# Kernel tuning notes

Measured on AMD Instinct MI355X. Metric: run time of the kernel, lower is better.

## Reference

```python
import jax, jax.numpy as jnp
import numpy as np

B, N_PER, F = 8, 4096, 64
RATIO, RADIUS, K = 0.25, 0.2, 64
S = int(N_PER * RATIO)  # 1024 samples per cloud
NEG = -1e30


def setup_inputs() -> dict:
    key = jax.random.key(0)
    ks = jax.random.split(key, 8)
    pos = jax.random.uniform(ks[0], (B * N_PER, 3), dtype=jnp.float32)
    x = jax.random.normal(ks[1], (B * N_PER, F), dtype=jnp.float32)
    batch = jnp.repeat(jnp.arange(B, dtype=jnp.int32), N_PER)
    W1 = jax.random.normal(ks[2], (F + 3, 128), dtype=jnp.float32) * 0.05
    b1 = jnp.zeros((128,), jnp.float32)
    W2 = jax.random.normal(ks[3], (128, 128), dtype=jnp.float32) * 0.05
    b2 = jnp.zeros((128,), jnp.float32)
    W3 = jax.random.normal(ks[4], (128, 256), dtype=jnp.float32) * 0.05
    b3 = jnp.zeros((256,), jnp.float32)
    return {"x": x, "pos": pos, "batch": batch,
            "W1": W1, "b1": b1, "W2": W2, "b2": b2, "W3": W3, "b3": b3}


def _fps_single(p):
    """Farthest point sampling on one cloud p:[N,3] -> S int32 indices (seed idx 0)."""
    d0 = jnp.sum((p - p[0]) ** 2, axis=-1)  # [N]

    def step(min_d, _):
        nxt = jnp.argmax(min_d).astype(jnp.int32)
        d = jnp.sum((p - p[nxt]) ** 2, axis=-1)
        return jnp.minimum(min_d, d), nxt

    _, rest = jax.lax.scan(step, d0, None, length=S - 1)
    return jnp.concatenate([jnp.zeros((1,), jnp.int32), rest])


def reference(x, pos, batch, W1, b1, W2, b2, W3, b3):
    pos_b = pos.reshape(B, N_PER, 3)
    x_b = x.reshape(B, N_PER, F)
    batch_b = batch.reshape(B, N_PER)

    # --- FPS sampling (sequential scan, vmapped over clouds) ---
    idx = jax.vmap(_fps_single)(pos_b)                                  # [B,S]
    pos_s = jnp.take_along_axis(pos_b, idx[..., None], axis=1)          # [B,S,3]

    # --- radius neighbor search: nearest K within RADIUS (deterministic) ---
    d2 = jnp.sum((pos_s[:, :, None, :] - pos_b[:, None, :, :]) ** 2, -1)  # [B,S,N]
    neg = jnp.where(d2 <= RADIUS ** 2, -d2, NEG)
    vals, nbr = jax.lax.top_k(neg, K)                                   # [B,S,K]
    valid = vals > NEG / 2                                              # [B,S,K]

    # --- gather neighbor features / positions ---
    x_j = jnp.take_along_axis(x_b[:, None], nbr[..., None], axis=2)     # [B,S,K,F]
    pos_j = jnp.take_along_axis(pos_b[:, None], nbr[..., None], axis=2) # [B,S,K,3]
    rel = pos_j - pos_s[:, :, None, :]                                  # [B,S,K,3]

    # --- edge MLP (Lin+ReLU per PyG PointNetConv local_nn) ---
    h = jnp.concatenate([x_j, rel], axis=-1)                            # [B,S,K,F+3]
    h = jax.nn.relu(h @ W1 + b1)
    h = jax.nn.relu(h @ W2 + b2)
    h = jax.nn.relu(h @ W3 + b3)                                        # [B,S,K,256]

    # --- scatter-max aggregation over neighbors ---
    h = jnp.where(valid[..., None], h, NEG)
    out = jnp.max(h, axis=2)                                            # [B,S,256]
    out = jnp.where(out > NEG / 2, out, 0.0)

    x1 = out.reshape(B * S, -1)
    pos1 = pos_s.reshape(B * S, 3)
    batch1 = jnp.take_along_axis(batch_b, idx, axis=1).reshape(-1)
    return x1, pos1, batch1
```

## Files before the change

kernel.cpp:

```cpp
#include <hip/hip_runtime.h>
#include <hip/hip_bf16.h>
#include <stdint.h>

#define NPER 4096
#define NCLOUD 8
#define FD 64
#define SS 1024
#define NBK 64
#define CAP 512

typedef unsigned int u32;
typedef unsigned long long u64;
typedef __attribute__((ext_vector_type(8))) short short8v;
typedef __attribute__((ext_vector_type(8))) unsigned short ushort8v;
typedef __attribute__((ext_vector_type(4))) float f32x4;

__device__ __forceinline__ float fadd(float a, float b){ return __fadd_rn(a,b); }
__device__ __forceinline__ float fsub(float a, float b){ return __fsub_rn(a,b); }
__device__ __forceinline__ float fmul(float a, float b){ return __fmul_rn(a,b); }
__device__ __forceinline__ float dist2(float ax,float ay,float az,float bx,float by,float bz){
  float dx=fsub(ax,bx), dy=fsub(ay,by), dz=fsub(az,bz);
  return fadd(fadd(fmul(dx,dx),fmul(dy,dy)),fmul(dz,dz));
}
__device__ __forceinline__ unsigned short f2b(float v){
  __hip_bfloat16 h = __float2bfloat16(v);
  return *reinterpret_cast<unsigned short*>(&h);
}

template<int CTRL, int RMASK>
__device__ __forceinline__ float dppmaxf(float v){
  int t = __builtin_amdgcn_update_dpp(0, __float_as_int(v), CTRL, RMASK, 0xf, false);
  return fmaxf(v, __int_as_float(t));
}

#define LOADG(q, j0, j1, j2, j3) { \
    const float4* pv = (const float4*)(pb + (size_t)(base + q*4)*3); \
    float4 v0=pv[0], v1=pv[1], v2=pv[2]; \
    x##j0=v0.x; y##j0=v0.y; z##j0=v0.z; \
    x##j1=v0.w; y##j1=v1.x; z##j1=v1.y; \
    x##j2=v1.z; y##j2=v1.w; z##j2=v2.x; \
    x##j3=v2.y; y##j3=v2.z; z##j3=v2.w; \
    float4 c0; c0.x=x##j0; c0.y=y##j0; c0.z=z##j0; c0.w=0.f; spt[base+q*4+0]=c0; \
    float4 c1; c1.x=x##j1; c1.y=y##j1; c1.z=z##j1; c1.w=0.f; spt[base+q*4+1]=c1; \
    float4 c2; c2.x=x##j2; c2.y=y##j2; c2.z=z##j2; c2.w=0.f; spt[base+q*4+2]=c2; \
    float4 c3; c3.x=x##j3; c3.y=y##j3; c3.z=z##j3; c3.w=0.f; spt[base+q*4+3]=c3; \
  }
#define DINIT(j) m##j = dist2(x##j,y##j,z##j,p0x,p0y,p0z);
#define DUPD(j)  { float d = dist2(x##j,y##j,z##j,pnx,pny,pnz); m##j = fminf(m##j,d); }
#define ARGMAX16() { \
      bool c; float w0,w1,w2,w3,w4,w5,w6,w7; int i0,i1,i2,i3,i4,i5,i6,i7; \
      c=m1>m0;   w0=c?m1:m0;   i0=base+(c?1:0); \
      c=m3>m2;   w1=c?m3:m2;   i1=base+(c?3:2); \
      c=m5>m4;   w2=c?m5:m4;   i2=base+(c?5:4); \
      c=m7>m6;   w3=c?m7:m6;   i3=base+(c?7:6); \
      c=m9>m8;   w4=c?m9:m8;   i4=base+(c?9:8); \
      c=m11>m10; w5=c?m11:m10; i5=base+(c?11:10); \
      c=m13>m12; w6=c?m13:m12; i6=base+(c?13:12); \
      c=m15>m14; w7=c?m15:m14; i7=base+(c?15:14); \
      c=w1>w0; w0=c?w1:w0; i0=c?i1:i0; \
      c=w3>w2; w2=c?w3:w2; i2=c?i3:i2; \
      c=w5>w4; w4=c?w5:w4; i4=c?i5:i4; \
      c=w7>w6; w6=c?w7:w6; i6=c?i7:i6; \
      c=w2>w0; w0=c?w2:w0; i0=c?i2:i0; \
      c=w6>w4; w4=c?w6:w4; i4=c?i6:i4; \
      c=w4>w0; bv=c?w4:w0; bidx=c?i4:i0; \
    }

__global__ __launch_bounds__(256, 1) void k_fps(const float* __restrict__ pos,
    float* __restrict__ pos_s, float* __restrict__ out_pos1, float* __restrict__ out_b1){
  __shared__ __align__(16) float4 spt[NPER];
  __shared__ __align__(16) u64 skey[2][4];
  const int b = blockIdx.x;
  const int t = threadIdx.x;
  const int w = t >> 6, lane = t & 63;
  const float* pb = pos + (size_t)b*NPER*3;
  const int base = t*16;
  float x0,x1,x2,x3,x4,x5,x6,x7,x8,x9,x10,x11,x12,x13,x14,x15;
  float y0,y1,y2,y3,y4,y5,y6,y7,y8,y9,y10,y11,y12,y13,y14,y15;
  float z0,z1,z2,z3,z4,z5,z6,z7,z8,z9,z10,z11,z12,z13,z14,z15;
  float m0,m1,m2,m3,m4,m5,m6,m7,m8,m9,m10,m11,m12,m13,m14,m15;
  LOADG(0, 0, 1, 2, 3)
  LOADG(1, 4, 5, 6, 7)
  LOADG(2, 8, 9, 10, 11)
  LOADG(3, 12, 13, 14, 15)
  const float p0x=pb[0], p0y=pb[1], p0z=pb[2];
  DINIT(0) DINIT(1) DINIT(2) DINIT(3) DINIT(4) DINIT(5) DINIT(6) DINIT(7)
  DINIT(8) DINIT(9) DINIT(10) DINIT(11) DINIT(12) DINIT(13) DINIT(14) DINIT(15)
  float bv; int bidx;
  ARGMAX16()
  float wx0=p0x, wy0=p0y, wz0=p0z;
  float wx1=0.f, wy1=0.f, wz1=0.f;
  float wx2=0.f, wy2=0.f, wz2=0.f;
  float wx3=0.f, wy3=0.f, wz3=0.f;
  for (int i=t;i<SS;i+=256) out_b1[b*SS+i] = (float)b;
  __syncthreads();
  auto fps_iter = [&](int it, float& wx, float& wy, float& wz) __attribute__((always_inline)) {
    float rv = bv;
    rv = dppmaxf<0x121,0xf>(rv);
    rv = dppmaxf<0x122,0xf>(rv);
    rv = dppmaxf<0x124,0xf>(rv);
    rv = dppmaxf<0x128,0xf>(rv);
    rv = dppmaxf<0x142,0xa>(rv);
    rv = dppmaxf<0x143,0xc>(rv);
    const float wv = __int_as_float(__builtin_amdgcn_readlane(__float_as_int(rv), 63));
    u64 em  = __ballot(bv == wv);
    u64 jb0 = __ballot((bidx & 1) != 0);
    u64 jb1 = __ballot((bidx & 2) != 0);
    u64 jb2 = __ballot((bidx & 4) != 0);
    u64 jb3 = __ballot((bidx & 8) != 0);
    const int wl = __ffsll(em) - 1;
    const int j  = (int)((jb0>>wl)&1) | ((int)((jb1>>wl)&1)<<1)
                 | ((int)((jb2>>wl)&1)<<2) | ((int)((jb3>>wl)&1)<<3);
    const int widx = (((w<<6)+wl)<<4) | j;
    const int par = it & 1;
    if (lane == 0)
      skey[par][w] = ((u64)__float_as_uint(wv)<<32) | (u64)(u32)(4095 - widx);
    __syncthreads();
    const u64* kp = &skey[par][0];
    u64 k0=kp[0], k1=kp[1], k2=kp[2], k3=kp[3];
    u64 ka = k0>k1?k0:k1, kb2 = k2>k3?k2:k3;
    u64 km = ka>kb2?ka:kb2;
    const int nxt = 4095 - (int)(km & 0xFFFull);
    const float4 c = spt[nxt];
    const float pnx = __int_as_float(__builtin_amdgcn_readfirstlane(__float_as_int(c.x)));
    const float pny = __int_as_float(__builtin_amdgcn_readfirstlane(__float_as_int(c.y)));
    const float pnz = __int_as_float(__builtin_amdgcn_readfirstlane(__float_as_int(c.z)));
    const bool mine = (t == (it & 255));
    wx = mine ? pnx : wx;
    wy = mine ? pny : wy;
    wz = mine ? pnz : wz;
    DUPD(0) DUPD(1) DUPD(2) DUPD(3) DUPD(4) DUPD(5) DUPD(6) DUPD(7)
    DUPD(8) DUPD(9) DUPD(10) DUPD(11) DUPD(12) DUPD(13) DUPD(14) DUPD(15)
    ARGMAX16()
  };
  for (int it=1;   it<256;  ++it) fps_iter(it, wx0, wy0, wz0);
  for (int it=256; it<512;  ++it) fps_iter(it, wx1, wy1, wz1);
  for (int it=512; it<768;  ++it) fps_iter(it, wx2, wy2, wz2);
  for (int it=768; it<1024; ++it) fps_iter(it, wx3, wy3, wz3);
  {
    const size_t g = (size_t)b*SS;
    size_t o = (g + t)*3;
    pos_s[o]=wx0; pos_s[o+1]=wy0; pos_s[o+2]=wz0;
    out_pos1[o]=wx0; out_pos1[o+1]=wy0; out_pos1[o+2]=wz0;
    o = (g + 256 + t)*3;
    pos_s[o]=wx1; pos_s[o+1]=wy1; pos_s[o+2]=wz1;
    out_pos1[o]=wx1; out_pos1[o+1]=wy1; out_pos1[o+2]=wz1;
    o = (g + 512 + t)*3;
    pos_s[o]=wx2; pos_s[o+1]=wy2; pos_s[o+2]=wz2;
    out_pos1[o]=wx2; out_pos1[o+1]=wy2; out_pos1[o+2]=wz2;
    o = (g + 768 + t)*3;
    pos_s[o]=wx3; pos_s[o+1]=wy3; pos_s[o+2]=wz3;
    out_pos1[o]=wx3; out_pos1[o+1]=wy3; out_pos1[o+2]=wz3;
  }
}

__global__ __launch_bounds__(256) void k_nbr(const float* __restrict__ pos,
    const float* __restrict__ pos_s, unsigned short* __restrict__ nbr){
  __shared__ float sxx[NPER], syy[NPER], szz[NPER];
  __shared__ u64 lst[4][CAP];
  __shared__ int cnt[4];
  const int t = threadIdx.x;
  const int w = t>>6, lane = t&63;
  const int gid0 = blockIdx.x*4;
  const int b = gid0 >> 10;
  const float* pb = pos + (size_t)b*NPER*3;
  for (int i=t;i<NPER;i+=256){
    sxx[i]=pb[i*3+0]; syy[i]=pb[i*3+1]; szz[i]=pb[i*3+2];
  }
  if (t<4) cnt[t]=0;
  __syncthreads();
  const int gid = gid0 + w;
  const float qx=pos_s[(size_t)gid*3+0], qy=pos_s[(size_t)gid*3+1], qz=pos_s[(size_t)gid*3+2];
  for (int i0=0;i0<NPER;i0+=64){
    int p = i0 + lane;
    float d = dist2(qx,qy,qz,sxx[p],syy[p],szz[p]);
    bool in = (d <= 0.04f);
    u64 m = __ballot(in);
    if (m){
      int tot = __popcll(m);
      int bse = 0;
      if (lane==0) bse = atomicAdd(&cnt[w], tot);
      bse = __shfl(bse, 0, 64);
      if (in){
        int o = bse + __popcll(m & ((1ull<<lane)-1ull));
        if (o < CAP) lst[w][o] = ((u64)__float_as_uint(d)<<12) | (u64)(u32)p;
      }
    }
  }
  int n = cnt[w];
  if (n > CAP) n = CAP;
  unsigned short outv = 0xFFFFu;
  if (n <= 64){
    if (lane < n) outv = (unsigned short)(lst[w][lane] & 0xFFFull);
  } else {
    for (int r=0;r<64;++r){
      u64 bk = ~0ull; int bp = -1;
      for (int i=lane;i<n;i+=64){
        u64 v = lst[w][i];
        bool lt = v < bk;
        bk = lt ? v : bk;
        bp = lt ? i : bp;
      }
      u64 rk = bk;
      #pragma unroll
      for (int off=32; off>=1; off>>=1){
        u64 o = __shfl_xor(rk, off, 64);
        rk = (o < rk) ? o : rk;
      }
      if (bk == rk) lst[w][bp] = ~0ull;
      if (lane == r) outv = (unsigned short)(rk & 0xFFFull);
    }
  }
  nbr[(size_t)gid*NBK + lane] = outv;
}

__global__ __launch_bounds__(256) void k_wconv(const float* __restrict__ W1,
    const float* __restrict__ W2, const float* __restrict__ W3,
    unsigned short* __restrict__ Wt1, unsigned short* __restrict__ Wt2,
    unsigned short* __restrict__ Wt3){
  int t = blockIdx.x*256 + threadIdx.x;
  if (t < 16384){
    int n = t>>7, k = t&127;
    Wt1[t] = f2b(k < 67 ? W1[k*128+n] : 0.f);
  } else if (t < 32768){
    int q = t - 16384; int n = q>>7, k = q&127;
    Wt2[q] = f2b(W2[k*128+n]);
  } else if (t < 65536){
    int q = t - 32768; int n = q>>7, k = q&127;
    Wt3[q] = f2b(W3[k*256+n]);
  }
}

__device__ __forceinline__ void load_w(const unsigned short* __restrict__ src,
    unsigned short* __restrict__ wb, int t){
  const int n = t>>1, hf = t&1;
  const char* srow = (const char*)(src + n*128 + hf*64);
  char* drow = (char*)wb + n*256;
  const u32 sw = (u32)(n&7)<<4;
  #pragma unroll
  for (int c=0;c<8;c++){
    ushort8v v = *(const ushort8v*)(srow + c*16);
    u32 colbyte = (u32)hf*128 + (u32)c*16;
    *(ushort8v*)(drow + (colbyte ^ sw)) = v;
  }
}

__device__ __forceinline__ void zero_acc(f32x4 acc[4][4]){
  #pragma unroll
  for (int i=0;i<4;i++){
    #pragma unroll
    for (int j=0;j<4;j++){
      f32x4 z = {0.f,0.f,0.f,0.f};
      acc[i][j] = z;
    }
  }
}

__device__ __forceinline__ void gemm_wave(const unsigned short* __restrict__ wb,
    const unsigned short* __restrict__ hb, int nh, int lane, int ksteps, f32x4 acc[4][4]){
  const int li = lane & 15;
  const int lg = lane >> 4;
  for (int kk=0; kk<ksteps; ++kk){
    const u32 colb = (u32)(kk*64 + lg*16);
    short8v af[4], bfv[4];
    #pragma unroll
    for (int mt=0;mt<4;mt++){
      int wr = nh*64 + mt*16 + li;
      af[mt] = *(const short8v*)((const char*)wb + wr*256 + (colb ^ ((u32)(wr&7)<<4)));
    }
    #pragma unroll
    for (int nt=0;nt<4;nt++){
      int er = nt*16 + li;
      bfv[nt] = *(const short8v*)((const char*)hb + er*256 + (colb ^ ((u32)(er&7)<<4)));
    }
    #pragma unroll
    for (int mt=0;mt<4;mt++){
      #pragma unroll
      for (int nt=0;nt<4;nt++){
        acc[mt][nt] = __builtin_amdgcn_mfma_f32_16x16x32_bf16(af[mt], bfv[nt], acc[mt][nt], 0, 0, 0);
      }
    }
  }
}

__device__ __forceinline__ void epi_store(f32x4 acc[4][4], const float* __restrict__ bias,
    unsigned short* __restrict__ hb, int nh, int lane){
  const int li = lane & 15;
  const int lg = lane >> 4;
  #pragma unroll
  for (int mt=0;mt<4;mt++){
    const int c0 = nh*64 + mt*16 + lg*4;
    const float4 bb = *(const float4*)(bias + c0);
    #pragma unroll
    for (int nt=0;nt<4;nt++){
      const int r = nt*16 + li;
      f32x4 a = acc[mt][nt];
      float v0 = fmaxf(a.x + bb.x, 0.f);
      float v1 = fmaxf(a.y + bb.y, 0.f);
      float v2 = fmaxf(a.z + bb.z, 0.f);
      float v3 = fmaxf(a.w + bb.w, 0.f);
      u64 pk = (u64)f2b(v0) | ((u64)f2b(v1)<<16) | ((u64)f2b(v2)<<32) | ((u64)f2b(v3)<<48);
      u32 colbyte = (u32)(c0*2);
      *(u64*)((char*)hb + r*256 + (colbyte ^ ((u32)(r&7)<<4))) = pk;
    }
  }
}

__device__ __forceinline__ void epi_out(f32x4 acc[4][4], const float* __restrict__ b3g,
    float* __restrict__ outx, u64 vmask, int pass, int nh, int lane, int gs){
  const int li = lane & 15;
  const int lg = lane >> 4;
  #pragma unroll
  for (int mt=0;mt<4;mt++){
    const int c0 = pass*128 + nh*64 + mt*16 + lg*4;
    const float4 bb = *(const float4*)(b3g + c0);
    float vals[4];
    #pragma unroll
    for (int i=0;i<4;i++){
      float v = -1e30f;
      #pragma unroll
      for (int nt=0;nt<4;nt++){
        const int r = nt*16 + li;
        const bool ok = (vmask >> r) & 1ull;
        const float a = acc[mt][nt][i];
        v = fmaxf(v, ok ? a : -1e30f);
      }
      #pragma unroll
      for (int off=1; off<16; off<<=1){
        v = fmaxf(v, __shfl_xor(v, off, 64));
      }
      float biasv = (i==0)?bb.x:((i==1)?bb.y:((i==2)?bb.z:bb.w));
      vals[i] = fmaxf(v + biasv, 0.f);
    }
    if (li==0){
      float4 o; o.x=vals[0]; o.y=vals[1]; o.z=vals[2]; o.w=vals[3];
      *(float4*)(outx + (size_t)gs*256 + c0) = o;
    }
  }
}

__global__ __launch_bounds__(256) void k_mlp(const float* __restrict__ xg,
    const float* __restrict__ pg, const float* __restrict__ pos_s,
    const unsigned short* __restrict__ nbrg,
    const unsigned short* __restrict__ Wt1, const unsigned short* __restrict__ Wt2,
    const unsigned short* __restrict__ Wt3,
    const float* __restrict__ b1g, const float* __restrict__ b2g,
    const float* __restrict__ b3g, float* __restrict__ outx){
  __shared__ __align__(16) unsigned short hbuf[2][64][128];
  __shared__ __align__(16) unsigned short wbuf[128*128];
  __shared__ float spos[2][4];
  __shared__ unsigned short snbr[2][64];
  __shared__ u64 svalid[2];
  const int t = threadIdx.x;
  const int s0 = blockIdx.x*2;
  const int b = s0 >> 10;
  {
    u64* p = (u64*)hbuf;
    #pragma unroll
    for (int i=0;i<16;i++) p[t + i*256] = 0ull;
  }
  if (t < 2){
    spos[t][0]=pos_s[(size_t)(s0+t)*3+0];
    spos[t][1]=pos_s[(size_t)(s0+t)*3+1];
    spos[t][2]=pos_s[(size_t)(s0+t)*3+2];
  }
  if (t < 128){
    const int s=t>>6, r=t&63;
    unsigned short nb = nbrg[(size_t)(s0+s)*NBK + r];
    snbr[s][r]=nb;
    u64 m = __ballot(nb != 0xFFFFu);
    if (r==0) svalid[s]=m;
  }
  __syncthreads();
  {
    const int s = t>>7, r=(t>>1)&63, hf=t&1;
    const unsigned short nb = snbr[s][r];
    char* drow = (char*)hbuf + (s*64+r)*256;
    const u32 sw = (u32)(r&7)<<4;
    if (nb != 0xFFFFu){
      const float4* xr = (const float4*)(xg + ((size_t)b*NPER + nb)*FD + hf*32);
      #pragma unroll
      for (int c=0;c<4;c++){
        float4 v0 = xr[2*c];
        float4 v1 = xr[2*c+1];
        ushort8v u;
        u[0]=f2b(v0.x); u[1]=f2b(v0.y); u[2]=f2b(v0.z); u[3]=f2b(v0.w);
        u[4]=f2b(v1.x); u[5]=f2b(v1.y); u[6]=f2b(v1.z); u[7]=f2b(v1.w);
        u32 colbyte = (u32)hf*64 + (u32)c*16;
        *(ushort8v*)(drow + (colbyte ^ sw)) = u;
      }
      if (hf){
        const size_t po = ((size_t)b*NPER + nb)*3;
        float rx = fsub(pg[po+0], spos[s][0]);
        float ry = fsub(pg[po+1], spos[s][1]);
        float rz = fsub(pg[po+2], spos[s][2]);
        u64 pk = (u64)f2b(rx) | ((u64)f2b(ry)<<16) | ((u64)f2b(rz)<<32);
        *(u64*)(drow + (128u ^ sw)) = pk;
      }
    }
  }
  load_w(Wt1, wbuf, t);
  __syncthreads();
  const int w = t>>6, lane = t&63;
  const int s = w>>1, nh = w&1;
  unsigned short* hb = &hbuf[s][0][0];
  f32x4 acc[4][4];
  zero_acc(acc);
  gemm_wave(wbuf, hb, nh, lane, 3, acc);
  __syncthreads();
  epi_store(acc, b1g, hb, nh, lane);
  load_w(Wt2, wbuf, t);
  __syncthreads();
  zero_acc(acc);
  gemm_wave(wbuf, hb, nh, lane, 4, acc);
  __syncthreads();
  epi_store(acc, b2g, hb, nh, lane);
  load_w(Wt3, wbuf, t);
  __syncthreads();
  zero_acc(acc);
  gemm_wave(wbuf, hb, nh, lane, 4, acc);
  const u64 vm = svalid[s];
  epi_out(acc, b3g, outx, vm, 0, nh, lane, s0+s);
  __syncthreads();
  load_w(Wt3 + 128*128, wbuf, t);
  __syncthreads();
  zero_acc(acc);
  gemm_wave(wbuf, hb, nh, lane, 4, acc);
  epi_out(acc, b3g, outx, vm, 1, nh, lane, s0+s);
}

extern "C" void kernel_launch(void* const* d_in, const int* in_sizes, int n_in,
                              void* d_out, int out_size, void* d_ws, size_t ws_size,
                              hipStream_t stream) {
  (void)in_sizes; (void)n_in; (void)out_size; (void)ws_size;
  const float* xg = (const float*)d_in[0];
  const float* pg = (const float*)d_in[1];
  const float* W1 = (const float*)d_in[3];
  const float* b1 = (const float*)d_in[4];
  const float* W2 = (const float*)d_in[5];
  const float* b2 = (const float*)d_in[6];
  const float* W3 = (const float*)d_in[7];
  const float* b3 = (const float*)d_in[8];
  float* outx = (float*)d_out;
  float* outp = outx + (size_t)8192*256;
  float* outb = outp + (size_t)8192*3;
  char* ws = (char*)d_ws;
  float* pos_s = (float*)ws;
  unsigned short* nbr = (unsigned short*)(ws + 98304);
  unsigned short* Wt1 = (unsigned short*)(ws + 98304 + 1048576);
  unsigned short* Wt2 = Wt1 + 16384;
  unsigned short* Wt3 = Wt2 + 16384;
  hipLaunchKernelGGL(k_fps, dim3(NCLOUD), dim3(256), 0, stream, pg, pos_s, outp, outb);
  hipLaunchKernelGGL(k_wconv, dim3(256), dim3(256), 0, stream, W1, W2, W3, Wt1, Wt2, Wt3);
  hipLaunchKernelGGL(k_nbr, dim3(8192/4), dim3(256), 0, stream, pg, pos_s, nbr);
  hipLaunchKernelGGL(k_mlp, dim3(8192/2), dim3(256), 0, stream,
                     xg, pg, pos_s, nbr, Wt1, Wt2, Wt3, b1, b2, b3, outx);
}
```

Before: 958.1 us.

## Pack FPS distance math into float2 ops and pass winner coords via small LDS slots

Rewrites the FPS kernel's per-point distance update to use 2-wide float vectors, so the compiler can emit packed FP32 instructions. It drops the full shared-memory point table. The winning lane in each wave now writes its own coordinates next to its key, and the cross-wave argmax is done with DPP on the four keys instead of serial LDS loads and a dependent coordinate lookup. This shortens the serial critical path of each of the 1023 FPS iterations, at the cost of extra select logic to pick the winner's coordinates from registers.

```diff
diff --git a/kernel.cpp b/kernel.cpp
--- a/kernel.cpp
+++ b/kernel.cpp
@@ -14,6 +14,7 @@
 typedef __attribute__((ext_vector_type(8))) short short8v;
 typedef __attribute__((ext_vector_type(8))) unsigned short ushort8v;
 typedef __attribute__((ext_vector_type(4))) float f32x4;
+typedef __attribute__((ext_vector_type(2))) float f32x2;
 
 __device__ __forceinline__ float fadd(float a, float b){ return __fadd_rn(a,b); }
 __device__ __forceinline__ float fsub(float a, float b){ return __fsub_rn(a,b); }
@@ -32,22 +33,37 @@
   int t = __builtin_amdgcn_update_dpp(0, __float_as_int(v), CTRL, RMASK, 0xf, false);
   return fmaxf(v, __int_as_float(t));
 }
-
-#define LOADG(q, j0, j1, j2, j3) { \
+template<int CTRL>
+__device__ __forceinline__ void kstage(u32& hi, u32& lo){
+  u32 hio = (u32)__builtin_amdgcn_update_dpp(0, (int)hi, CTRL, 0xf, 0xf, false);
+  u32 loo = (u32)__builtin_amdgcn_update_dpp(0, (int)lo, CTRL, 0xf, 0xf, false);
+  u64 ko = ((u64)hio<<32)|loo, k = ((u64)hi<<32)|lo;
+  bool g = ko > k;
+  hi = g?hio:hi; lo = g?loo:lo;
+}
+
+#define LOADQ(q, pA, pB) { \
     const float4* pv = (const float4*)(pb + (size_t)(base + q*4)*3); \
     float4 v0=pv[0], v1=pv[1], v2=pv[2]; \
-    x##j0=v0.x; y##j0=v0.y; z##j0=v0.z; \
-    x##j1=v0.w; y##j1=v1.x; z##j1=v1.y; \
-    x##j2=v1.z; y##j2=v1.w; z##j2=v2.x; \
-    x##j3=v2.y; y##j3=v2.z; z##j3=v2.w; \
-    float4 c0; c0.x=x##j0; c0.y=y##j0; c0.z=z##j0; c0.w=0.f; spt[base+q*4+0]=c0; \
-    float4 c1; c1.x=x##j1; c1.y=y##j1; c1.z=z##j1; c1.w=0.f; spt[base+q*4+1]=c1; \
-    float4 c2; c2.x=x##j2; c2.y=y##j2; c2.z=z##j2; c2.w=0.f; spt[base+q*4+2]=c2; \
-    float4 c3; c3.x=x##j3; c3.y=y##j3; c3.z=z##j3; c3.w=0.f; spt[base+q*4+3]=c3; \
-  }
-#define DINIT(j) m##j = dist2(x##j,y##j,z##j,p0x,p0y,p0z);
-#define DUPD(j)  { float d = dist2(x##j,y##j,z##j,pnx,pny,pnz); m##j = fminf(m##j,d); }
-#define ARGMAX16() { \
+    ax##pA[0]=v0.x; ay##pA[0]=v0.y; az##pA[0]=v0.z; \
+    ax##pA[1]=v0.w; ay##pA[1]=v1.x; az##pA[1]=v1.y; \
+    ax##pB[0]=v1.z; ay##pB[0]=v1.w; az##pB[0]=v2.x; \
+    ax##pB[1]=v2.y; ay##pB[1]=v2.z; az##pB[1]=v2.w; \
+  }
+#define DINITP(p) { \
+    f32x2 dx = ax##p - px2, dy = ay##p - py2, dz = az##p - pz2; \
+    f32x2 s = dx*dx, ss = dy*dy, tt = dz*dz; \
+    s = s + ss; am##p = s + tt; }
+#define DUPDP(p) { \
+    f32x2 dx = ax##p - px2, dy = ay##p - py2, dz = az##p - pz2; \
+    f32x2 s = dx*dx, ss = dy*dy, tt = dz*dz; \
+    s = s + ss; s = s + tt; \
+    am##p = __builtin_elementwise_min(am##p, s); }
+#define ARGMAX16P() { \
+      float m0=am0[0],m1=am0[1],m2=am1[0],m3=am1[1]; \
+      float m4=am2[0],m5=am2[1],m6=am3[0],m7=am3[1]; \
+      float m8=am4[0],m9=am4[1],m10=am5[0],m11=am5[1]; \
+      float m12=am6[0],m13=am6[1],m14=am7[0],m15=am7[1]; \
       bool c; float w0,w1,w2,w3,w4,w5,w6,w7; int i0,i1,i2,i3,i4,i5,i6,i7; \
       c=m1>m0;   w0=c?m1:m0;   i0=base+(c?1:0); \
       c=m3>m2;   w1=c?m3:m2;   i1=base+(c?3:2); \
@@ -65,29 +81,41 @@
       c=w6>w4; w4=c?w6:w4; i4=c?i6:i4; \
       c=w4>w0; bv=c?w4:w0; bidx=c?i4:i0; \
     }
+#define SELP(r, a0,a1,a2,a3,a4,a5,a6,a7) { \
+      float e0=(j&1)?a0[1]:a0[0], e1=(j&1)?a1[1]:a1[0]; \
+      float e2=(j&1)?a2[1]:a2[0], e3=(j&1)?a3[1]:a3[0]; \
+      float e4=(j&1)?a4[1]:a4[0], e5=(j&1)?a5[1]:a5[0]; \
+      float e6=(j&1)?a6[1]:a6[0], e7=(j&1)?a7[1]:a7[0]; \
+      float f0=(j&2)?e1:e0, f1=(j&2)?e3:e2, f2=(j&2)?e5:e4, f3=(j&2)?e7:e6; \
+      float g0=(j&4)?f1:f0, g1=(j&4)?f3:f2; \
+      r=(j&8)?g1:g0; }
 
 __global__ __launch_bounds__(256, 1) void k_fps(const float* __restrict__ pos,
     float* __restrict__ pos_s, float* __restrict__ out_pos1, float* __restrict__ out_b1){
-  __shared__ __align__(16) float4 spt[NPER];
-  __shared__ __align__(16) u64 skey[2][4];
+#pragma clang fp contract(off)
+  __shared__ __align__(16) u64   skey[2][4];
+  __shared__ __align__(16) float scoor[2][4][4];
   const int b = blockIdx.x;
   const int t = threadIdx.x;
   const int w = t >> 6, lane = t & 63;
   const float* pb = pos + (size_t)b*NPER*3;
   const int base = t*16;
-  float x0,x1,x2,x3,x4,x5,x6,x7,x8,x9,x10,x11,x12,x13,x14,x15;
-  float y0,y1,y2,y3,y4,y5,y6,y7,y8,y9,y10,y11,y12,y13,y14,y15;
-  float z0,z1,z2,z3,z4,z5,z6,z7,z8,z9,z10,z11,z12,z13,z14,z15;
-  float m0,m1,m2,m3,m4,m5,m6,m7,m8,m9,m10,m11,m12,m13,m14,m15;
-  LOADG(0, 0, 1, 2, 3)
-  LOADG(1, 4, 5, 6, 7)
-  LOADG(2, 8, 9, 10, 11)
-  LOADG(3, 12, 13, 14, 15)
+  f32x2 ax0,ax1,ax2,ax3,ax4,ax5,ax6,ax7;
+  f32x2 ay0,ay1,ay2,ay3,ay4,ay5,ay6,ay7;
+  f32x2 az0,az1,az2,az3,az4,az5,az6,az7;
+  f32x2 am0,am1,am2,am3,am4,am5,am6,am7;
+  LOADQ(0, 0, 1)
+  LOADQ(1, 2, 3)
+  LOADQ(2, 4, 5)
+  LOADQ(3, 6, 7)
   const float p0x=pb[0], p0y=pb[1], p0z=pb[2];
-  DINIT(0) DINIT(1) DINIT(2) DINIT(3) DINIT(4) DINIT(5) DINIT(6) DINIT(7)
-  DINIT(8) DINIT(9) DINIT(10) DINIT(11) DINIT(12) DINIT(13) DINIT(14) DINIT(15)
+  {
+    f32x2 px2={p0x,p0x}, py2={p0y,p0y}, pz2={p0z,p0z};
+    DINITP(0) DINITP(1) DINITP(2) DINITP(3)
+    DINITP(4) DINITP(5) DINITP(6) DINITP(7)
+  }
   float bv; int bidx;
-  ARGMAX16()
+  ARGMAX16P()
   float wx0=p0x, wy0=p0y, wz0=p0z;
   float wx1=0.f, wy1=0.f, wz1=0.f;
   float wx2=0.f, wy2=0.f, wz2=0.f;
@@ -112,26 +140,37 @@
     const int j  = (int)((jb0>>wl)&1) | ((int)((jb1>>wl)&1)<<1)
                  | ((int)((jb2>>wl)&1)<<2) | ((int)((jb3>>wl)&1)<<3);
     const int widx = (((w<<6)+wl)<<4) | j;
+    float xw, yw, zw;
+    SELP(xw, ax0,ax1,ax2,ax3,ax4,ax5,ax6,ax7)
+    SELP(yw, ay0,ay1,ay2,ay3,ay4,ay5,ay6,ay7)
+    SELP(zw, az0,az1,az2,az3,az4,az5,az6,az7)
     const int par = it & 1;
-    if (lane == 0)
+    if (lane == wl){
       skey[par][w] = ((u64)__float_as_uint(wv)<<32) | (u64)(u32)(4095 - widx);
+      float4 c; c.x=xw; c.y=yw; c.z=zw; c.w=0.f;
+      *(float4*)&scoor[par][w][0] = c;
+    }
     __syncthreads();
-    const u64* kp = &skey[par][0];
-    u64 k0=kp[0], k1=kp[1], k2=kp[2], k3=kp[3];
-    u64 ka = k0>k1?k0:k1, kb2 = k2>k3?k2:k3;
-    u64 km = ka>kb2?ka:kb2;
-    const int nxt = 4095 - (int)(km & 0xFFFull);
-    const float4 c = spt[nxt];
-    const float pnx = __int_as_float(__builtin_amdgcn_readfirstlane(__float_as_int(c.x)));
-    const float pny = __int_as_float(__builtin_amdgcn_readfirstlane(__float_as_int(c.y)));
-    const float pnz = __int_as_float(__builtin_amdgcn_readfirstlane(__float_as_int(c.z)));
+    u64 k = skey[par][lane & 3];
+    const float4 cc = *(const float4*)&scoor[par][lane & 3][0];
+    u32 hi = (u32)(k>>32), lo = (u32)k;
+    kstage<0x121>(hi,lo);
+    kstage<0x122>(hi,lo);
+    const int rec = (4095 - (int)(lo & 0xFFFu)) >> 10;
+    const int sr  = __builtin_amdgcn_readfirstlane(rec);
+    const float pnx = __int_as_float(__builtin_amdgcn_readlane(__float_as_int(cc.x), sr));
+    const float pny = __int_as_float(__builtin_amdgcn_readlane(__float_as_int(cc.y), sr));
+    const float pnz = __int_as_float(__builtin_amdgcn_readlane(__float_as_int(cc.z), sr));
     const bool mine = (t == (it & 255));
     wx = mine ? pnx : wx;
     wy = mine ? pny : wy;
     wz = mine ? pnz : wz;
-    DUPD(0) DUPD(1) DUPD(2) DUPD(3) DUPD(4) DUPD(5) DUPD(6) DUPD(7)
-    DUPD(8) DUPD(9) DUPD(10) DUPD(11) DUPD(12) DUPD(13) DUPD(14) DUPD(15)
-    ARGMAX16()
+    {
+      f32x2 px2={pnx,pnx}, py2={pny,pny}, pz2={pnz,pnz};
+      DUPDP(0) DUPDP(1) DUPDP(2) DUPDP(3)
+      DUPDP(4) DUPDP(5) DUPDP(6) DUPDP(7)
+    }
+    ARGMAX16P()
   };
   for (int it=1;   it<256;  ++it) fps_iter(it, wx0, wy0, wz0);
   for (int it=256; it<512;  ++it) fps_iter(it, wx1, wy1, wz1);
```

Result: slower. 1.372 ms (+43.2%).
